# Kernel optimization log

Hardware: AMD Instinct MI355X
Metric: run time of the kernel (lower is better)

## Reference

```python
import jax, jax.numpy as jnp
import numpy as np

N = 100000
C = 128
VEC = 16
GRID = 128
TEMP = 1.0
REP = C // VEC


def _offsets_cube():
    r = [-1, 0, 1]
    return np.array([[i, j, k] for i in r for j in r for k in r], dtype=np.int64)


def _offsets_cross(d):
    offs = [[0, 0, 0]]
    for ax in range(3):
        for s in (-d, d):
            o = [0, 0, 0]
            o[ax] = s
            offs.append(o)
    return np.array(offs, dtype=np.int64)


def _build_nbr(coords, lut, offs):
    # coords [N,3] int, lut: flat grid -> voxel idx or -1. Returns [K,N] int32, -1 = missing.
    maps = []
    for o in offs:
        nc = coords + o
        valid = np.all((nc >= 0) & (nc < GRID), axis=1)
        flat = nc[:, 0] * GRID * GRID + nc[:, 1] * GRID + nc[:, 2]
        idx = np.where(valid, lut[np.clip(flat, 0, GRID ** 3 - 1)], -1)
        maps.append(idx)
    return jnp.asarray(np.stack(maps).astype(np.int32))


def setup_inputs() -> dict:
    rng = np.random.default_rng(0)
    flat = rng.choice(GRID ** 3, size=N, replace=False)
    coords = np.stack([flat // (GRID * GRID), (flat // GRID) % GRID, flat % GRID], axis=1)
    lut = np.full(GRID ** 3, -1, dtype=np.int64)
    lut[flat] = np.arange(N)
    nbr_cross2 = _build_nbr(coords, lut, _offsets_cross(2))  # expert 0: HYPER_CROSS dil=2, K=7
    nbr_cube = _build_nbr(coords, lut, _offsets_cube())       # expert 1: HYPER_CUBE dil=1, K=27
    nbr_cross3 = _build_nbr(coords, lut, _offsets_cross(3))  # expert 2: HYPER_CROSS dil=3, K=7

    ks = jax.random.split(jax.random.key(0), 10)
    s = lambda k, shape, sc: jax.random.normal(k, shape, jnp.float32) * sc
    return dict(
        x=s(ks[0], (N, C), 1.0),
        v1_w=s(ks[1], (27, C, C), 0.05),
        v1_g=jnp.ones((C,), jnp.float32), v1_b=jnp.zeros((C,), jnp.float32),
        v2_w=s(ks[2], (C, C), 0.05),
        v2_g=jnp.ones((C,), jnp.float32), v2_b=jnp.zeros((C,), jnp.float32),
        q_w=s(ks[3], (C, VEC), 0.05),
        q_g=jnp.ones((VEC,), jnp.float32), q_b=jnp.zeros((VEC,), jnp.float32),
        cb0=s(ks[4], (7, C), 0.1),
        cb1=s(ks[5], (27, C), 0.1),
        cb2=s(ks[6], (7, C), 0.1),
        out_w=s(ks[7], (C, C), 0.05),
        out_g=jnp.ones((C,), jnp.float32), out_b=jnp.zeros((C,), jnp.float32),
        nbr_cross2=nbr_cross2, nbr_cube=nbr_cube, nbr_cross3=nbr_cross3,
    )


def _bn(x, g, b, eps=1e-5):
    m = x.mean(0)
    v = x.var(0)
    return (x - m) * jax.lax.rsqrt(v + eps) * g + b


def _sparse_conv(x, nbr, W):
    # full sparse conv: out[i] = sum_k W[k] @ x[nbr[k,i]] over valid neighbors
    out = jnp.zeros((x.shape[0], W.shape[2]), x.dtype)
    for k in range(W.shape[0]):  # fixed small K, structural loop
        idx = nbr[k]
        g = jnp.where((idx >= 0)[:, None], x[jnp.clip(idx, 0)], 0.0)
        out = out + g @ W[k]
    return out


def _chanwise_conv(x, nbr, kern):
    # MinkowskiChannelwiseConvolution: out[i,c] = sum_k kern[k,c] * x[nbr[k,i],c]
    out = jnp.zeros_like(x)
    for k in range(kern.shape[0]):
        idx = nbr[k]
        out = out + jnp.where((idx >= 0)[:, None], x[jnp.clip(idx, 0)], 0.0) * kern[k]
    return out


def _pairwise_score(q, nbr):
    # pairwise qk: mean over valid neighbors j of q_i * q_j (per channel) -> [N, VEC]
    acc = jnp.zeros_like(q)
    cnt = jnp.zeros((q.shape[0], 1), q.dtype)
    for k in range(nbr.shape[0]):
        idx = nbr[k]
        valid = (idx >= 0)[:, None]
        acc = acc + jnp.where(valid, q[jnp.clip(idx, 0)], 0.0)
        cnt = cnt + valid.astype(q.dtype)
    return q * acc / jnp.maximum(cnt, 1.0)


def reference(x, v1_w, v1_g, v1_b, v2_w, v2_g, v2_b, q_w, q_g, q_b,
              cb0, cb1, cb2, out_w, out_g, out_b,
              nbr_cross2, nbr_cube, nbr_cross3):
    # value branch: 3x3 ConvBNReLU -> 1x1 ConvBNReLU
    v = jax.nn.relu(_bn(_sparse_conv(x, nbr_cube, v1_w), v1_g, v1_b))
    v = jax.nn.relu(_bn(v @ v2_w, v2_g, v2_b))
    # query: 1x1 ConvBNReLU -> [N, VEC]
    q = jax.nn.relu(_bn(x @ q_w, q_g, q_b))
    # M=3 channelwise codebook expert convs on the value features
    cb_outs = [
        _chanwise_conv(v, nbr_cross2, cb0),
        _chanwise_conv(v, nbr_cube, cb1),
        _chanwise_conv(v, nbr_cross3, cb2),
    ]
    # pairwise attention scores per expert neighborhood -> [N, VEC, M]
    scores = jnp.stack([
        _pairwise_score(q, nbr_cross2),
        _pairwise_score(q, nbr_cube),
        _pairwise_score(q, nbr_cross3),
    ], axis=-1)
    attn = jax.nn.softmax(scores / TEMP, axis=-1)
    attn = jnp.repeat(attn, REP, axis=1)  # expand_vec_dim: [N, C, M]
    out = sum(attn[:, :, m] * cb_outs[m] for m in range(3))
    out = jax.nn.relu(_bn(out @ out_w, out_g, out_b))
    return out + x  # residual (inplanes == planes, downsample is identity)
```

## Files before the change

kernel.cpp:

```cpp
#include <hip/hip_runtime.h>

#define NN 100000
#define C 128
#define VEC 16
#define AROW 136
#define GCAP 240000

typedef __bf16 bfx8 __attribute__((ext_vector_type(8)));
typedef float f32x4 __attribute__((ext_vector_type(4)));

__device__ inline unsigned pack_bf2(float a, float b) {
    unsigned ua = __float_as_uint(a);
    unsigned ub = __float_as_uint(b);
    ua = (ua + 0x7fffu + ((ua >> 16) & 1u)) >> 16;
    ub = (ub + 0x7fffu + ((ub >> 16) & 1u)) >> 16;
    return ua | (ub << 16);
}
__device__ inline unsigned short bf1(float a) {
    unsigned u = __float_as_uint(a);
    return (unsigned short)((u + 0x7fffu + ((u >> 16) & 1u)) >> 16);
}

__device__ inline void wconv_body(const float* __restrict__ W, unsigned short* __restrict__ Wf, int F) {
    int e = F & 7, l = (F >> 3) & 63, nt = (F >> 9) & 7, ks = (F >> 12) & 3, kt = F >> 14;
    int cin = ks * 32 + (l >> 4) * 8 + e;
    int cout = nt * 16 + (l & 15);
    Wf[F] = bf1(W[((size_t)kt * C + cin) * C + cout]);
}

__global__ __launch_bounds__(256) void prep(const float* __restrict__ v1w, const float* __restrict__ v2w,
                                            const float* __restrict__ outw,
                                            unsigned short* __restrict__ v1f, unsigned short* __restrict__ v2f,
                                            unsigned short* __restrict__ outf) {
    int b = blockIdx.x, tid = threadIdx.x;
    if (b < 1728)       wconv_body(v1w, v1f, b * 256 + tid);
    else if (b < 1792)  wconv_body(v2w, v2f, (b - 1728) * 256 + tid);
    else                wconv_body(outw, outf, (b - 1792) * 256 + tid);
}

__global__ __launch_bounds__(256) void compactA(const int* __restrict__ nbr, int* __restrict__ cnt,
                                                int* __restrict__ slotmap, int* __restrict__ pairs,
                                                unsigned* __restrict__ maskbuf) {
    const int k = blockIdx.x / 49, cb = blockIdx.x % 49, tid = threadIdx.x;
    const int i0 = cb * 2048 + tid * 8;
    int j[8]; int lc = 0;
#pragma unroll
    for (int t = 0; t < 8; ++t) {
        int i = i0 + t;
        j[t] = (i < NN) ? nbr[(size_t)k * NN + i] : -1;
        lc += (j[t] >= 0);
    }
    __shared__ int ls[256]; __shared__ int sbase;
    ls[tid] = lc; __syncthreads();
    for (int off = 1; off < 256; off <<= 1) {
        int v = (tid >= off) ? ls[tid - off] : 0;
        __syncthreads();
        ls[tid] += v;
        __syncthreads();
    }
    if (tid == 255) sbase = atomicAdd(&cnt[k], ls[255]);
// ... 3 lines not shown
        int i = i0 + t; if (i >= NN) break;
        int s = -1;
        if (j[t] >= 0) {
            s = slot++;
            pairs[(size_t)k * NN + s] = j[t];
            atomicOr(&maskbuf[i], 1u << k);
        }
        slotmap[(size_t)k * NN + i] = s;
    }
}

__global__ void prefixA2(int* __restrict__ hdr) {
    if (threadIdx.x == 0) {
        int co = 0, go = 0;
        for (int k = 0; k < 27; ++k) {
            hdr[32 + k] = co; hdr[64 + k] = go;
            int nch = (hdr[k] + 31) / 32;
            co += nch; go += nch * 32;
        }
        hdr[32 + 27] = co;
    }
}

__global__ __launch_bounds__(256) void convB(const float* __restrict__ x, const int* __restrict__ pairs,
                                             const int* __restrict__ hdr, const bfx8* __restrict__ Wf,
                                             unsigned short* __restrict__ g) {
    const int tid = threadIdx.x, l = tid & 63, w = tid >> 6, rr = tid >> 4, gg = tid & 15;
    __shared__ int sco[28], scnt[27], sgo[27];
    __shared__ unsigned short Ash[32 * AROW];
    __shared__ unsigned short Osh[32 * AROW];
    if (tid < 28) sco[tid] = hdr[32 + tid];
    if (tid < 27) { scnt[tid] = hdr[tid]; sgo[tid] = hdr[64 + tid]; }
    __syncthreads();
    const int tot = sco[27];
    for (int t = blockIdx.x; t < tot; t += gridDim.x) {
        int lo = 0, hi = 26;
        while (lo < hi) { int mid = (lo + hi + 1) >> 1; if (sco[mid] <= t) lo = mid; else hi = mid - 1; }
        const int k = lo, c = t - sco[k], cntk = scnt[k];
        const int srow = c * 32;
        const size_t gbase = (size_t)(sgo[k] + srow) * C;
#pragma unroll
        for (int h = 0; h < 2; ++h) {
            int row = srow + h * 16 + rr;
            uint4 pk = {0u, 0u, 0u, 0u};
            if (row < cntk) {
                int j = pairs[(size_t)k * NN + row];
                const float* xr = x + (size_t)j * C + gg * 8;
                float4 xa = *reinterpret_cast<const float4*>(xr);
                float4 xb = *reinterpret_cast<const float4*>(xr + 4);
                pk.x = pack_bf2(xa.x, xa.y); pk.y = pack_bf2(xa.z, xa.w);
                pk.z = pack_bf2(xb.x, xb.y); pk.w = pack_bf2(xb.z, xb.w);
            }
            *reinterpret_cast<uint4*>(&Ash[(h * 16 + rr) * AROW + gg * 8]) = pk;
        }
        __syncthreads();
        f32x4 a00 = {0.f,0.f,0.f,0.f}, a01 = {0.f,0.f,0.f,0.f};
        f32x4 a10 = {0.f,0.f,0.f,0.f}, a11 = {0.f,0.f,0.f,0.f};
        const unsigned short* ar0 = &Ash[(l & 15) * AROW + (l >> 4) * 8];
        const unsigned short* ar1 = &Ash[(16 + (l & 15)) * AROW + (l >> 4) * 8];
#pragma unroll
        for (int ks = 0; ks < 4; ++ks) {
            bfx8 b0 = Wf[((k * 4 + ks) * 8 + 2 * w) * 64 + l];
            bfx8 b1 = Wf[((k * 4 + ks) * 8 + 2 * w + 1) * 64 + l];
            bfx8 f0 = *reinterpret_cast<const bfx8*>(ar0 + ks * 32);
            bfx8 f1 = *reinterpret_cast<const bfx8*>(ar1 + ks * 32);
            a00 = __builtin_amdgcn_mfma_f32_16x16x32_bf16(f0, b0, a00, 0, 0, 0);
            a01 = __builtin_amdgcn_mfma_f32_16x16x32_bf16(f0, b1, a01, 0, 0, 0);
            a10 = __builtin_amdgcn_mfma_f32_16x16x32_bf16(f1, b0, a10, 0, 0, 0);
            a11 = __builtin_amdgcn_mfma_f32_16x16x32_bf16(f1, b1, a11, 0, 0, 0);
        }
#pragma unroll
        for (int r = 0; r < 4; ++r) {
            int row = (l >> 4) * 4 + r;
            Osh[row * AROW + w * 32 + (l & 15)]        = bf1(a00[r]);
// ... 30 lines not shown
        const unsigned short* gr = &g[(size_t)(sgo[k] + slot) * C + c0];
        uint4 u = *reinterpret_cast<const uint4*>(gr);
        acc[0] += __uint_as_float(u.x << 16); acc[1] += __uint_as_float(u.x & 0xffff0000u);
        acc[2] += __uint_as_float(u.y << 16); acc[3] += __uint_as_float(u.y & 0xffff0000u);
        acc[4] += __uint_as_float(u.z << 16); acc[5] += __uint_as_float(u.z & 0xffff0000u);
        acc[6] += __uint_as_float(u.w << 16); acc[7] += __uint_as_float(u.w & 0xffff0000u);
    }
#pragma unroll
    for (int c2 = 0; c2 < 8; ++c2) outt[p * 132 + c0 + c2] = acc[c2];
    uint4 pk;
    pk.x = pack_bf2(acc[0], acc[1]); pk.y = pack_bf2(acc[2], acc[3]);
    pk.z = pack_bf2(acc[4], acc[5]); pk.w = pack_bf2(acc[6], acc[7]);
    *reinterpret_cast<uint4*>(&outh[(size_t)i * C + c0]) = pk;
    __syncthreads();
    if (tid < 128) {
        float s = 0.f, q = 0.f;
#pragma unroll
        for (int r = 0; r < 16; ++r) { float v = outt[r * 132 + tid]; s += v; q += v * v; }
        psb[(size_t)blockIdx.x * C + tid] = s;
        pqb[(size_t)blockIdx.x * C + tid] = q;
    }
}

__global__ __launch_bounds__(256) void mm_bn_h(const unsigned short* __restrict__ in,
                                               const float* __restrict__ a,
                                               const float* __restrict__ cc,
                                               int dorelu,
                                               const bfx8* __restrict__ Wf,
                                               unsigned short* __restrict__ out,
                                               float* __restrict__ psb,
                                               float* __restrict__ pqb) {
    const int tid = threadIdx.x, l = tid & 63, w = tid >> 6;
    const int rr = tid >> 4, gg = tid & 15;
    const size_t base = (size_t)blockIdx.x * 16;
    __shared__ unsigned short Ash[16 * AROW];
    __shared__ float outt[16 * 132];
    {
        uint4 u = *reinterpret_cast<const uint4*>(in + (base + rr) * C + gg * 8);
        if (dorelu) {
            float4 a4 = *reinterpret_cast<const float4*>(&a[gg * 8]);
            float4 a4b = *reinterpret_cast<const float4*>(&a[gg * 8 + 4]);
            float4 c4 = *reinterpret_cast<const float4*>(&cc[gg * 8]);
            float4 c4b = *reinterpret_cast<const float4*>(&cc[gg * 8 + 4]);
            float e0 = fmaxf(fmaf(__uint_as_float(u.x << 16),        a4.x,  c4.x), 0.f);
            float e1 = fmaxf(fmaf(__uint_as_float(u.x & 0xffff0000u), a4.y,  c4.y), 0.f);
            float e2 = fmaxf(fmaf(__uint_as_float(u.y << 16),        a4.z,  c4.z), 0.f);
            float e3 = fmaxf(fmaf(__uint_as_float(u.y & 0xffff0000u), a4.w,  c4.w), 0.f);
            float e4 = fmaxf(fmaf(__uint_as_float(u.z << 16),        a4b.x, c4b.x), 0.f);
            float e5 = fmaxf(fmaf(__uint_as_float(u.z & 0xffff0000u), a4b.y, c4b.y), 0.f);
            float e6 = fmaxf(fmaf(__uint_as_float(u.w << 16),        a4b.z, c4b.z), 0.f);
            float e7 = fmaxf(fmaf(__uint_as_float(u.w & 0xffff0000u), a4b.w, c4b.w), 0.f);
            u.x = pack_bf2(e0, e1); u.y = pack_bf2(e2, e3);
            u.z = pack_bf2(e4, e5); u.w = pack_bf2(e6, e7);
        }
        *reinterpret_cast<uint4*>(&Ash[rr * AROW + gg * 8]) = u;
    }
    __syncthreads();
    f32x4 acc0 = {0.f, 0.f, 0.f, 0.f};
    f32x4 acc1 = {0.f, 0.f, 0.f, 0.f};
    const unsigned short* arow = &Ash[(l & 15) * AROW + (l >> 4) * 8];
#pragma unroll
    for (int ks = 0; ks < 4; ++ks) {
        bfx8 af = *reinterpret_cast<const bfx8*>(arow + ks * 32);
        bfx8 b0 = Wf[(ks * 8 + 2 * w) * 64 + l];
        bfx8 b1 = Wf[(ks * 8 + 2 * w + 1) * 64 + l];
        acc0 = __builtin_amdgcn_mfma_f32_16x16x32_bf16(af, b0, acc0, 0, 0, 0);
        acc1 = __builtin_amdgcn_mfma_f32_16x16x32_bf16(af, b1, acc1, 0, 0, 0);
    }
#pragma unroll
    for (int r = 0; r < 4; ++r) {
        int row = (l >> 4) * 4 + r;
        outt[row * 132 + w * 32 + (l & 15)] = acc0[r];
        outt[row * 132 + w * 32 + 16 + (l & 15)] = acc1[r];
    }
    __syncthreads();
    {
        float4 v0 = *reinterpret_cast<float4*>(&outt[rr * 132 + gg * 8]);
        float4 v1 = *reinterpret_cast<float4*>(&outt[rr * 132 + gg * 8 + 4]);
        uint4 pk;
        pk.x = pack_bf2(v0.x, v0.y); pk.y = pack_bf2(v0.z, v0.w);
        pk.z = pack_bf2(v1.x, v1.y); pk.w = pack_bf2(v1.z, v1.w);
        *reinterpret_cast<uint4*>(&out[(base + rr) * C + gg * 8]) = pk;
    }
    if (tid < 128) {
        float s = 0.f, q = 0.f;
#pragma unroll
        for (int r = 0; r < 16; ++r) { float v = outt[r * 132 + tid]; s += v; q += v * v; }
        psb[(size_t)blockIdx.x * C + tid] = s;
        pqb[(size_t)blockIdx.x * C + tid] = q;
    }
}

__global__ __launch_bounds__(256) void qmm(const float* __restrict__ x,
                                           const float* __restrict__ qw,
                                           float* __restrict__ outq) {
    const int v = threadIdx.x & 15, p = threadIdx.x >> 4;
    const size_t i = (size_t)blockIdx.x * 16 + p;
    float acc = 0.f;
    for (int cin0 = 0; cin0 < C; cin0 += 4) {
        float4 xv = *reinterpret_cast<const float4*>(x + i * C + cin0);
        acc += xv.x * qw[(cin0 + 0) * VEC + v] + xv.y * qw[(cin0 + 1) * VEC + v]
             + xv.z * qw[(cin0 + 2) * VEC + v] + xv.w * qw[(cin0 + 3) * VEC + v];
    }
    outq[i * VEC + v] = acc;
}

__global__ __launch_bounds__(256) void stats_mid128(const float* __restrict__ psb,
                                                    const float* __restrict__ pqb,
                                                    int rows,
                                                    float* __restrict__ ps2,
                                                    float* __restrict__ pq2) {
    const int ch = threadIdx.x & 127, half = threadIdx.x >> 7;
    float s = 0.f, q = 0.f;
    for (int i = blockIdx.x * 2 + half; i < rows; i += 128) {
        s += psb[(size_t)i * C + ch];
        q += pqb[(size_t)i * C + ch];
    }
    __shared__ float ls[256], lq[256];
    ls[threadIdx.x] = s; lq[threadIdx.x] = q;
    __syncthreads();
    if (threadIdx.x < 128) {
        ps2[blockIdx.x * C + ch] = ls[threadIdx.x] + ls[threadIdx.x + 128];
        pq2[blockIdx.x * C + ch] = lq[threadIdx.x] + lq[threadIdx.x + 128];
    }
}

__global__ __launch_bounds__(256) void stats_partial16(const float* __restrict__ buf,
                                                       float* __restrict__ ps,
                                                       float* __restrict__ pq) {
    const int ch = threadIdx.x & 15, grp = threadIdx.x >> 4;
    float s = 0.f, q = 0.f;
    for (int i = blockIdx.x * 16 + grp; i < NN; i += gridDim.x * 16) {
        float val = buf[(size_t)i * VEC + ch];
        s += val; q += val * val;
    }
    __shared__ float ls[256], lq[256];
    ls[threadIdx.x] = s; lq[threadIdx.x] = q;
    __syncthreads();
    if (threadIdx.x < 16) {
        float ss = 0.f, qq = 0.f;
        for (int g2 = 0; g2 < 16; ++g2) { ss += ls[g2 * 16 + ch]; qq += lq[g2 * 16 + ch]; }
        ps[blockIdx.x * VEC + ch] = ss; pq[blockIdx.x * VEC + ch] = qq;
    }
}

__global__ void stats_final(const float* __restrict__ ps, const float* __restrict__ pq,
                            int nb, int cdim,
                            const float* __restrict__ g, const float* __restrict__ b,
                            float* __restrict__ a, float* __restrict__ cc) {
    int ch = threadIdx.x;
    if (ch >= cdim) return;
    float s = 0.f, q = 0.f;
    for (int i = 0; i < nb; ++i) { s += ps[i * cdim + ch]; q += pq[i * cdim + ch]; }
    float m = s / (float)NN;
    float var = q / (float)NN - m * m;
    var = fmaxf(var, 0.f);
    float rs = rsqrtf(var + 1e-5f);
    float av = g[ch] * rs;
    a[ch] = av;
    cc[ch] = b[ch] - m * av;
}

__global__ __launch_bounds__(256) void bn_relu_ip(float* __restrict__ buf,
                                                  const float* __restrict__ a,
                                                  const float* __restrict__ cc,
                                                  int total4, int mask) {
    for (int t = blockIdx.x * blockDim.x + threadIdx.x; t < total4; t += gridDim.x * blockDim.x) {
        float4 v = reinterpret_cast<float4*>(buf)[t];
        int ch = (t * 4) & mask;
        v.x = fmaxf(fmaf(v.x, a[ch + 0], cc[ch + 0]), 0.f);
        v.y = fmaxf(fmaf(v.y, a[ch + 1], cc[ch + 1]), 0.f);
        v.z = fmaxf(fmaf(v.z, a[ch + 2], cc[ch + 2]), 0.f);
        v.w = fmaxf(fmaf(v.w, a[ch + 3], cc[ch + 3]), 0.f);
        reinterpret_cast<float4*>(buf)[t] = v;
    }
}

__global__ __launch_bounds__(256) void bnrelu_h(const unsigned short* __restrict__ in,
                                                const float* __restrict__ a,
                                                const float* __restrict__ cc,
                                                unsigned short* __restrict__ outh) {
    const int total8 = NN * C / 8;
    for (int t = blockIdx.x * 256 + threadIdx.x; t < total8; t += gridDim.x * 256) {
        int ch = (t * 8) & 127;
        uint4 u = *reinterpret_cast<const uint4*>(in + (size_t)t * 8);
        float4 a4 = *reinterpret_cast<const float4*>(&a[ch]);
        float4 a4b = *reinterpret_cast<const float4*>(&a[ch + 4]);
        float4 c4 = *reinterpret_cast<const float4*>(&cc[ch]);
        float4 c4b = *reinterpret_cast<const float4*>(&cc[ch + 4]);
        float e0 = fmaxf(fmaf(__uint_as_float(u.x << 16),        a4.x,  c4.x), 0.f);
        float e1 = fmaxf(fmaf(__uint_as_float(u.x & 0xffff0000u), a4.y,  c4.y), 0.f);
        float e2 = fmaxf(fmaf(__uint_as_float(u.y << 16),        a4.z,  c4.z), 0.f);
        float e3 = fmaxf(fmaf(__uint_as_float(u.y & 0xffff0000u), a4.w,  c4.w), 0.f);
        float e4 = fmaxf(fmaf(__uint_as_float(u.z << 16),        a4b.x, c4b.x), 0.f);
        float e5 = fmaxf(fmaf(__uint_as_float(u.z & 0xffff0000u), a4b.y, c4b.y), 0.f);
        float e6 = fmaxf(fmaf(__uint_as_float(u.w << 16),        a4b.z, c4b.z), 0.f);
        float e7 = fmaxf(fmaf(__uint_as_float(u.w & 0xffff0000u), a4b.w, c4b.w), 0.f);
        uint4 pk;
        pk.x = pack_bf2(e0, e1); pk.y = pack_bf2(e2, e3);
        pk.z = pack_bf2(e4, e5); pk.w = pack_bf2(e6, e7);
        *reinterpret_cast<uint4*>(&outh[(size_t)t * 8]) = pk;
    }
}

__global__ __launch_bounds__(256) void attn_fused16c(const unsigned short* __restrict__ vbf,
                                                     const float* __restrict__ qbuf,
                                                     const int* __restrict__ nA,
                                                     const int* __restrict__ nB,
                                                     const int* __restrict__ nC,
                                                     const float* __restrict__ cb0,
                                                     const float* __restrict__ cb1,
                                                     const float* __restrict__ cb2,
                                                     unsigned short* __restrict__ outm) {
    const int tid = threadIdx.x;
    const int base = blockIdx.x * 16;
    __shared__ int raw[16][41];
    __shared__ int sj[16][44];
    __shared__ short sk[16][44];
    __shared__ short sb[16][4];
    __shared__ float sattn[16][16][3];

    for (int t = tid; t < 656; t += 256) {
        int k = t >> 4, p = t & 15;
        int i = base + p;
        int j;
        if (k < 7)       j = nA[(size_t)k * NN + i];
        else if (k < 34) j = nB[(size_t)(k - 7) * NN + i];
        else             j = nC[(size_t)(k - 34) * NN + i];
        raw[p][k] = j;
    }
    __syncthreads();
    if (tid < 16) {
        int p = tid, n = 0;
#pragma unroll
        for (int k = 0; k < 7; ++k) { int j = raw[p][k]; if (j >= 0) { sj[p][n] = j; sk[p][n] = (short)k; ++n; } }
        int b0 = n;
#pragma unroll
        for (int k = 7; k < 34; ++k) { int j = raw[p][k]; if (j >= 0) { sj[p][n] = j; sk[p][n] = (short)(k - 7); ++n; } }
        int b1 = n;
#pragma unroll
        for (int k = 34; k < 41; ++k) { int j = raw[p][k]; if (j >= 0) { sj[p][n] = j; sk[p][n] = (short)(k - 34); ++n; } }
        sb[p][0] = (short)b0; sb[p][1] = (short)b1; sb[p][2] = (short)n;
    }
    __syncthreads();
    {
        int p = tid >> 4, v = tid & 15;
        int b0 = sb[p][0], b1 = sb[p][1], b2 = sb[p][2];
        float qi = qbuf[(size_t)(base + p) * VEC + v];
        float a0 = 0.f, a1 = 0.f, a2 = 0.f;
        for (int s = 0; s < b0; ++s) a0 += qbuf[(size_t)sj[p][s] * VEC + v];
        for (int s = b0; s < b1; ++s) a1 += qbuf[(size_t)sj[p][s] * VEC + v];
        for (int s = b1; s < b2; ++s) a2 += qbuf[(size_t)sj[p][s] * VEC + v];
        float s0 = qi * a0 / (float)(b0 > 0 ? b0 : 1);
        float s1 = qi * a1 / (float)(b1 - b0 > 0 ? b1 - b0 : 1);
        float s2 = qi * a2 / (float)(b2 - b1 > 0 ? b2 - b1 : 1);
        float mx = fmaxf(s0, fmaxf(s1, s2));
        float e0 = __expf(s0 - mx), e1 = __expf(s1 - mx), e2 = __expf(s2 - mx);
        float inv = 1.f / (e0 + e1 + e2);
        sattn[p][v][0] = e0 * inv; sattn[p][v][1] = e1 * inv; sattn[p][v][2] = e2 * inv;
    }
    __syncthreads();
    {
        int p = tid >> 4, g = tid & 15, c0 = g * 8;
        int b0 = sb[p][0], b1 = sb[p][1], b2 = sb[p][2];
        float A0[8], A1[8], A2[8];
#pragma unroll
        for (int c = 0; c < 8; ++c) { A0[c] = 0.f; A1[c] = 0.f; A2[c] = 0.f; }
        for (int s = 0; s < b0; ++s) {
            int j = sj[p][s], k = sk[p][s];
            uint4 u = *reinterpret_cast<const uint4*>(vbf + (size_t)j * C + c0);
            float4 ca = *reinterpret_cast<const float4*>(&cb0[k * C + c0]);
            float4 cb = *reinterpret_cast<const float4*>(&cb0[k * C + c0 + 4]);
            A0[0] = fmaf(ca.x, __uint_as_float(u.x << 16), A0[0]);
            A0[1] = fmaf(ca.y, __uint_as_float(u.x & 0xffff0000u), A0[1]);
            A0[2] = fmaf(ca.z, __uint_as_float(u.y << 16), A0[2]);
            A0[3] = fmaf(ca.w, __uint_as_float(u.y & 0xffff0000u), A0[3]);
            A0[4] = fmaf(cb.x, __uint_as_float(u.z << 16), A0[4]);
            A0[5] = fmaf(cb.y, __uint_as_float(u.z & 0xffff0000u), A0[5]);
            A0[6] = fmaf(cb.z, __uint_as_float(u.w << 16), A0[6]);
            A0[7] = fmaf(cb.w, __uint_as_float(u.w & 0xffff0000u), A0[7]);
        }
        for (int s = b0; s < b1; ++s) {
            int j = sj[p][s], k = sk[p][s];
            uint4 u = *reinterpret_cast<const uint4*>(vbf + (size_t)j * C + c0);
            float4 ca = *reinterpret_cast<const float4*>(&cb1[k * C + c0]);
            float4 cb = *reinterpret_cast<const float4*>(&cb1[k * C + c0 + 4]);
            A1[0] = fmaf(ca.x, __uint_as_float(u.x << 16), A1[0]);
            A1[1] = fmaf(ca.y, __uint_as_float(u.x & 0xffff0000u), A1[1]);
            A1[2] = fmaf(ca.z, __uint_as_float(u.y << 16), A1[2]);
            A1[3] = fmaf(ca.w, __uint_as_float(u.y & 0xffff0000u), A1[3]);
            A1[4] = fmaf(cb.x, __uint_as_float(u.z << 16), A1[4]);
            A1[5] = fmaf(cb.y, __uint_as_float(u.z & 0xffff0000u), A1[5]);
            A1[6] = fmaf(cb.z, __uint_as_float(u.w << 16), A1[6]);
            A1[7] = fmaf(cb.w, __uint_as_float(u.w & 0xffff0000u), A1[7]);
        }
        for (int s = b1; s < b2; ++s) {
            int j = sj[p][s], k = sk[p][s];
            uint4 u = *reinterpret_cast<const uint4*>(vbf + (size_t)j * C + c0);
            float4 ca = *reinterpret_cast<const float4*>(&cb2[k * C + c0]);
            float4 cb = *reinterpret_cast<const float4*>(&cb2[k * C + c0 + 4]);
            A2[0] = fmaf(ca.x, __uint_as_float(u.x << 16), A2[0]);
            A2[1] = fmaf(ca.y, __uint_as_float(u.x & 0xffff0000u), A2[1]);
            A2[2] = fmaf(ca.z, __uint_as_float(u.y << 16), A2[2]);
            A2[3] = fmaf(ca.w, __uint_as_float(u.y & 0xffff0000u), A2[3]);
            A2[4] = fmaf(cb.x, __uint_as_float(u.z << 16), A2[4]);
            A2[5] = fmaf(cb.y, __uint_as_float(u.z & 0xffff0000u), A2[5]);
            A2[6] = fmaf(cb.z, __uint_as_float(u.w << 16), A2[6]);
            A2[7] = fmaf(cb.w, __uint_as_float(u.w & 0xffff0000u), A2[7]);
        }
        float w0 = sattn[p][g][0], w1 = sattn[p][g][1], w2 = sattn[p][g][2];
        float o[8];
#pragma unroll
        for (int c = 0; c < 8; ++c) o[c] = w0 * A0[c] + w1 * A1[c] + w2 * A2[c];
        uint4 pk;
        pk.x = pack_bf2(o[0], o[1]); pk.y = pack_bf2(o[2], o[3]);
        pk.z = pack_bf2(o[4], o[5]); pk.w = pack_bf2(o[6], o[7]);
        *reinterpret_cast<uint4*>(&outm[(size_t)(base + p) * C + c0]) = pk;
    }
}

__global__ __launch_bounds__(256) void final_bn_res_h(const unsigned short* __restrict__ buf,
                                                      const float* __restrict__ a,
                                                      const float* __restrict__ cc,
                                                      const float* __restrict__ x,
                                                      float* __restrict__ out) {
    const int total8 = NN * C / 8;
    for (int t = blockIdx.x * 256 + threadIdx.x; t < total8; t += gridDim.x * 256) {
        int ch = (t * 8) & 127;
        uint4 u = *reinterpret_cast<const uint4*>(buf + (size_t)t * 8);
        float4 xa = *reinterpret_cast<const float4*>(x + (size_t)t * 8);
        float4 xb = *reinterpret_cast<const float4*>(x + (size_t)t * 8 + 4);
// ... 28 lines not shown
    const float* v2_b = (const float*)d_in[6];
    const float* q_w  = (const float*)d_in[7];
    const float* q_g  = (const float*)d_in[8];
    const float* q_b  = (const float*)d_in[9];
    const float* cb0  = (const float*)d_in[10];
    const float* cb1  = (const float*)d_in[11];
    const float* cb2  = (const float*)d_in[12];
    const float* out_w = (const float*)d_in[13];
    const float* out_g = (const float*)d_in[14];
    const float* out_b = (const float*)d_in[15];
    const int* nbrA = (const int*)d_in[16];
    const int* nbrB = (const int*)d_in[17];
    const int* nbrC = (const int*)d_in[18];
    float* out = (float*)d_out;

    float* w = (float*)d_ws;
    unsigned short* bufAh = (unsigned short*)w;
    float* r1 = w + (size_t)NN * C / 2;
    unsigned short* g = (unsigned short*)r1;
    int* slotmap = (int*)(r1 + 15360000);
    int* pairs   = (int*)(r1 + 15360000 + 2700000);
    unsigned short* bufBh = (unsigned short*)r1;
    float* bufQ = r1 + 6400000;
    unsigned short* vbf = (unsigned short*)(r1 + 6400000 + 1600000);
    size_t o = (size_t)NN * C / 2 + 20760000;
    float* psb  = w + o; o += (size_t)6250 * C;
    float* pqb  = w + o; o += (size_t)6250 * C;
    float* ps2  = w + o; o += 64 * C;
    float* pq2  = w + o; o += 64 * C;
    float* ps16 = w + o; o += 128 * VEC;
    float* pq16 = w + o; o += 128 * VEC;
    float* a1 = w + o; o += C;  float* c1 = w + o; o += C;
    float* a2 = w + o; o += C;  float* c2 = w + o; o += C;
    float* ao = w + o; o += C;  float* co = w + o; o += C;
    float* aq = w + o; o += VEC; float* cq = w + o; o += VEC;
    unsigned short* v1f = (unsigned short*)(w + o); o += (27 * 16384) / 2;
    unsigned short* v2f = (unsigned short*)(w + o); o += 16384 / 2;
    unsigned short* outf = (unsigned short*)(w + o); o += 16384 / 2;
    int* hdr = (int*)(w + o); o += 128;
    unsigned* maskbuf = (unsigned*)(w + o); o += NN;

    const int total4q = NN * VEC / 4;

    hipMemsetAsync(hdr, 0, (size_t)(128 + NN) * sizeof(int), stream);
    prep<<<1856, 256, 0, stream>>>(v1_w, v2_w, out_w, v1f, v2f, outf);

    compactA<<<27 * 49, 256, 0, stream>>>(nbrB, hdr, slotmap, pairs, maskbuf);
    prefixA2<<<1, 64, 0, stream>>>(hdr);
    convB<<<2048, 256, 0, stream>>>(x, pairs, hdr, (const bfx8*)v1f, g);
    convC<<<NN / 16, 256, 0, stream>>>(g, slotmap, hdr, maskbuf, bufAh, psb, pqb);
    stats_mid128<<<64, 256, 0, stream>>>(psb, pqb, 6250, ps2, pq2);
    stats_final<<<1, 128, 0, stream>>>(ps2, pq2, 64, C, v1_g, v1_b, a1, c1);

    mm_bn_h<<<NN / 16, 256, 0, stream>>>(bufAh, a1, c1, 1, (const bfx8*)v2f, bufBh, psb, pqb);
    stats_mid128<<<64, 256, 0, stream>>>(psb, pqb, 6250, ps2, pq2);
    stats_final<<<1, 128, 0, stream>>>(ps2, pq2, 64, C, v2_g, v2_b, a2, c2);

    bnrelu_h<<<2048, 256, 0, stream>>>(bufBh, a2, c2, vbf);

    qmm<<<NN / 16, 256, 0, stream>>>(x, q_w, bufQ);
    stats_partial16<<<128, 256, 0, stream>>>(bufQ, ps16, pq16);
    stats_final<<<1, 64, 0, stream>>>(ps16, pq16, 128, VEC, q_g, q_b, aq, cq);
    bn_relu_ip<<<1024, 256, 0, stream>>>(bufQ, aq, cq, total4q, 15);

    attn_fused16c<<<NN / 16, 256, 0, stream>>>(vbf, bufQ, nbrA, nbrB, nbrC, cb0, cb1, cb2, bufAh);

    mm_bn_h<<<NN / 16, 256, 0, stream>>>(bufAh, nullptr, nullptr, 0, (const bfx8*)outf, bufBh, psb, pqb);
    stats_mid128<<<64, 256, 0, stream>>>(psb, pqb, 6250, ps2, pq2);
    stats_final<<<1, 128, 0, stream>>>(ps2, pq2, 64, C, out_g, out_b, ao, co);
    final_bn_res_h<<<2048, 256, 0, stream>>>(bufBh, ao, co, x, out);
}
```

Measured before the change: 389.9 us.

## Pre-convert x to bf16, fuse BN stats finalisation, fold BN-ReLU into attention

Converts x to bf16 once inside the prep kernel, so the conv gather reads half the bytes and skips repacking on every reuse. The two-stage BN statistics reduction becomes a single kernel that uses an atomic ticket to let the last block finalise. The separate BN+ReLU passes on the value and query features are folded into the attention kernel's loads. The 1x1 matmul kernel now handles 32 rows per block, and the three expert loops in attention are merged into one loop with a branch per element. This removes several launches and full-tensor passes, at the cost of extra bf16 workspace, repeated BN math per gathered neighbour, and a divergent branch in the inner loop.

```diff
diff --git a/kernel.cpp b/kernel.cpp
--- a/kernel.cpp
+++ b/kernel.cpp
@@ -29,13 +29,24 @@
 }
 
 __global__ __launch_bounds__(256) void prep(const float* __restrict__ v1w, const float* __restrict__ v2w,
-                                            const float* __restrict__ outw,
+                                            const float* __restrict__ outw, const float* __restrict__ x,
                                             unsigned short* __restrict__ v1f, unsigned short* __restrict__ v2f,
-                                            unsigned short* __restrict__ outf) {
+                                            unsigned short* __restrict__ outf, unsigned short* __restrict__ xh) {
     int b = blockIdx.x, tid = threadIdx.x;
     if (b < 1728)       wconv_body(v1w, v1f, b * 256 + tid);
     else if (b < 1792)  wconv_body(v2w, v2f, (b - 1728) * 256 + tid);
-    else                wconv_body(outw, outf, (b - 1792) * 256 + tid);
+    else if (b < 1856)  wconv_body(outw, outf, (b - 1792) * 256 + tid);
+    else {
+        const int total8 = NN * C / 8;
+        for (int t = (b - 1856) * 256 + tid; t < total8; t += 1024 * 256) {
+            float4 xa = *reinterpret_cast<const float4*>(x + (size_t)t * 8);
+            float4 xb = *reinterpret_cast<const float4*>(x + (size_t)t * 8 + 4);
+            uint4 pk;
+            pk.x = pack_bf2(xa.x, xa.y); pk.y = pack_bf2(xa.z, xa.w);
+            pk.z = pack_bf2(xb.x, xb.y); pk.w = pack_bf2(xb.z, xb.w);
+            *reinterpret_cast<uint4*>(&xh[(size_t)t * 8]) = pk;
+        }
+    }
 }
 
 __global__ __launch_bounds__(256) void compactA(const int* __restrict__ nbr, int* __restrict__ cnt,
@@ -85,7 +96,7 @@
     }
 }
 
-__global__ __launch_bounds__(256) void convB(const float* __restrict__ x, const int* __restrict__ pairs,
+__global__ __launch_bounds__(256) void convB(const unsigned short* __restrict__ xh, const int* __restrict__ pairs,
                                              const int* __restrict__ hdr, const bfx8* __restrict__ Wf,
                                              unsigned short* __restrict__ g) {
     const int tid = threadIdx.x, l = tid & 63, w = tid >> 6, rr = tid >> 4, gg = tid & 15;
@@ -108,11 +119,7 @@
             uint4 pk = {0u, 0u, 0u, 0u};
             if (row < cntk) {
                 int j = pairs[(size_t)k * NN + row];
-                const float* xr = x + (size_t)j * C + gg * 8;
-                float4 xa = *reinterpret_cast<const float4*>(xr);
-                float4 xb = *reinterpret_cast<const float4*>(xr + 4);
-                pk.x = pack_bf2(xa.x, xa.y); pk.y = pack_bf2(xa.z, xa.w);
-                pk.z = pack_bf2(xb.x, xb.y); pk.w = pack_bf2(xb.z, xb.w);
+                pk = *reinterpret_cast<const uint4*>(xh + (size_t)j * C + gg * 8);
             }
             *reinterpret_cast<uint4*>(&Ash[(h * 16 + rr) * AROW + gg * 8]) = pk;
         }
@@ -189,21 +196,99 @@
     }
 }
 
-__global__ __launch_bounds__(256) void mm_bn_h(const unsigned short* __restrict__ in,
-                                               const float* __restrict__ a,
-                                               const float* __restrict__ cc,
-                                               int dorelu,
-                                               const bfx8* __restrict__ Wf,
-                                               unsigned short* __restrict__ out,
-                                               float* __restrict__ psb,
-                                               float* __restrict__ pqb) {
+__global__ __launch_bounds__(256) void statsF128(const float* __restrict__ psb, const float* __restrict__ pqb,
+                                                 int rows,
+                                                 float* __restrict__ ps2, float* __restrict__ pq2,
+                                                 const float* __restrict__ g, const float* __restrict__ b,
+                                                 float* __restrict__ a, float* __restrict__ cc,
+                                                 int* __restrict__ ticket) {
+    const int tid = threadIdx.x, ch = tid & 127, half = tid >> 7;
+    float s = 0.f, q = 0.f;
+    for (int i = blockIdx.x * 2 + half; i < rows; i += 128) {
+        s += psb[(size_t)i * C + ch];
+        q += pqb[(size_t)i * C + ch];
+    }
+    __shared__ float ls[256], lq[256];
+    __shared__ int amlast;
+    ls[tid] = s; lq[tid] = q;
+    __syncthreads();
+    if (tid < 128) {
+        ps2[blockIdx.x * C + ch] = ls[tid] + ls[tid + 128];
+        pq2[blockIdx.x * C + ch] = lq[tid] + lq[tid + 128];
+    }
+    __threadfence();
+    __syncthreads();
+    if (tid == 0) amlast = (atomicAdd(ticket, 1) == 63) ? 1 : 0;
+    __syncthreads();
+    if (!amlast) return;
+    __threadfence();
+    if (tid < 128) {
+        float ss = 0.f, qq = 0.f;
+        for (int i = 0; i < 64; ++i) { ss += ps2[i * C + ch]; qq += pq2[i * C + ch]; }
+        float m = ss / (float)NN;
+        float var = fmaxf(qq / (float)NN - m * m, 0.f);
+        float rs = rsqrtf(var + 1e-5f);
+        float av = g[ch] * rs;
+        a[ch] = av;
+        cc[ch] = b[ch] - m * av;
+    }
+}
+
+__global__ __launch_bounds__(256) void statsF16(const float* __restrict__ buf,
+                                                float* __restrict__ ps2, float* __restrict__ pq2,
+                                                const float* __restrict__ g, const float* __restrict__ b,
+                                                float* __restrict__ a, float* __restrict__ cc,
+                                                int* __restrict__ ticket) {
+    const int tid = threadIdx.x, ch = tid & 15, grp = tid >> 4;
+    float s = 0.f, q = 0.f;
+    for (int i = blockIdx.x * 16 + grp; i < NN; i += 64 * 16) {
+        float val = buf[(size_t)i * VEC + ch];
+        s += val; q += val * val;
+    }
+    __shared__ float ls[256], lq[256];
+    __shared__ int amlast;
+    ls[tid] = s; lq[tid] = q;
+    __syncthreads();
+    if (tid < 16) {
+        float ss = 0.f, qq = 0.f;
+        for (int g2 = 0; g2 < 16; ++g2) { ss += ls[g2 * 16 + ch]; qq += lq[g2 * 16 + ch]; }
+        ps2[blockIdx.x * VEC + ch] = ss; pq2[blockIdx.x * VEC + ch] = qq;
+    }
+    __threadfence();
+    __syncthreads();
+    if (tid == 0) amlast = (atomicAdd(ticket, 1) == 63) ? 1 : 0;
+    __syncthreads();
+    if (!amlast) return;
+    __threadfence();
+    if (tid < 16) {
+        float ss = 0.f, qq = 0.f;
+        for (int i = 0; i < 64; ++i) { ss += ps2[i * VEC + ch]; qq += pq2[i * VEC + ch]; }
+        float m = ss / (float)NN;
+        float var = fmaxf(qq / (float)NN - m * m, 0.f);
+        float rs = rsqrtf(var + 1e-5f);
+        float av = g[ch] * rs;
+        a[ch] = av;
+        cc[ch] = b[ch] - m * av;
+    }
+}
+
+__global__ __launch_bounds__(256) void mm_bn_h32(const unsigned short* __restrict__ in,
+                                                 const float* __restrict__ a,
+                                                 const float* __restrict__ cc,
+                                                 int dorelu,
+                                                 const bfx8* __restrict__ Wf,
+                                                 unsigned short* __restrict__ out,
+                                                 float* __restrict__ psb,
+                                                 float* __restrict__ pqb) {
     const int tid = threadIdx.x, l = tid & 63, w = tid >> 6;
     const int rr = tid >> 4, gg = tid & 15;
-    const size_t base = (size_t)blockIdx.x * 16;
-    __shared__ unsigned short Ash[16 * AROW];
-    __shared__ float outt[16 * 132];
-    {
-        uint4 u = *reinterpret_cast<const uint4*>(in + (base + rr) * C + gg * 8);
+    const size_t base = (size_t)blockIdx.x * 32;
+    __shared__ unsigned short Ash[32 * AROW];
+    __shared__ float outt[32 * 132];
+#pragma unroll
+    for (int h = 0; h < 2; ++h) {
+        int row = h * 16 + rr;
+        uint4 u = *reinterpret_cast<const uint4*>(in + (base + row) * C + gg * 8);
         if (dorelu) {
             float4 a4 = *reinterpret_cast<const float4*>(&a[gg * 8]);
             float4 a4b = *reinterpret_cast<const float4*>(&a[gg * 8 + 4]);
@@ -220,39 +305,47 @@
             u.x = pack_bf2(e0, e1); u.y = pack_bf2(e2, e3);
             u.z = pack_bf2(e4, e5); u.w = pack_bf2(e6, e7);
         }
-        *reinterpret_cast<uint4*>(&Ash[rr * AROW + gg * 8]) = u;
-    }
-    __syncthreads();
-    f32x4 acc0 = {0.f, 0.f, 0.f, 0.f};
-    f32x4 acc1 = {0.f, 0.f, 0.f, 0.f};
-    const unsigned short* arow = &Ash[(l & 15) * AROW + (l >> 4) * 8];
+        *reinterpret_cast<uint4*>(&Ash[row * AROW + gg * 8]) = u;
+    }
+    __syncthreads();
+    f32x4 a00 = {0.f,0.f,0.f,0.f}, a01 = {0.f,0.f,0.f,0.f};
+    f32x4 a10 = {0.f,0.f,0.f,0.f}, a11 = {0.f,0.f,0.f,0.f};
+    const unsigned short* ar0 = &Ash[(l & 15) * AROW + (l >> 4) * 8];
+    const unsigned short* ar1 = &Ash[(16 + (l & 15)) * AROW + (l >> 4) * 8];
 #pragma unroll
     for (int ks = 0; ks < 4; ++ks) {
-        bfx8 af = *reinterpret_cast<const bfx8*>(arow + ks * 32);
         bfx8 b0 = Wf[(ks * 8 + 2 * w) * 64 + l];
         bfx8 b1 = Wf[(ks * 8 + 2 * w + 1) * 64 + l];
-        acc0 = __builtin_amdgcn_mfma_f32_16x16x32_bf16(af, b0, acc0, 0, 0, 0);
-        acc1 = __builtin_amdgcn_mfma_f32_16x16x32_bf16(af, b1, acc1, 0, 0, 0);
+        bfx8 f0 = *reinterpret_cast<const bfx8*>(ar0 + ks * 32);
+        bfx8 f1 = *reinterpret_cast<const bfx8*>(ar1 + ks * 32);
+        a00 = __builtin_amdgcn_mfma_f32_16x16x32_bf16(f0, b0, a00, 0, 0, 0);
+        a01 = __builtin_amdgcn_mfma_f32_16x16x32_bf16(f0, b1, a01, 0, 0, 0);
+        a10 = __builtin_amdgcn_mfma_f32_16x16x32_bf16(f1, b0, a10, 0, 0, 0);
+        a11 = __builtin_amdgcn_mfma_f32_16x16x32_bf16(f1, b1, a11, 0, 0, 0);
     }
 #pragma unroll
     for (int r = 0; r < 4; ++r) {
         int row = (l >> 4) * 4 + r;
-        outt[row * 132 + w * 32 + (l & 15)] = acc0[r];
-        outt[row * 132 + w * 32 + 16 + (l & 15)] = acc1[r];
-    }
-    __syncthreads();
-    {
-        float4 v0 = *reinterpret_cast<float4*>(&outt[rr * 132 + gg * 8]);
-        float4 v1 = *reinterpret_cast<float4*>(&outt[rr * 132 + gg * 8 + 4]);
+        outt[row * 132 + w * 32 + (l & 15)]        = a00[r];
+        outt[row * 132 + w * 32 + 16 + (l & 15)]   = a01[r];
+        outt[(16 + row) * 132 + w * 32 + (l & 15)] = a10[r];
+        outt[(16 + row) * 132 + w * 32 + 16 + (l & 15)] = a11[r];
+    }
+    __syncthreads();
+#pragma unroll
+    for (int h = 0; h < 2; ++h) {
+        int row = h * 16 + rr;
+        float4 v0 = *reinterpret_cast<float4*>(&outt[row * 132 + gg * 8]);
+        float4 v1 = *reinterpret_cast<float4*>(&outt[row * 132 + gg * 8 + 4]);
         uint4 pk;
         pk.x = pack_bf2(v0.x, v0.y); pk.y = pack_bf2(v0.z, v0.w);
         pk.z = pack_bf2(v1.x, v1.y); pk.w = pack_bf2(v1.z, v1.w);
-        *reinterpret_cast<uint4*>(&out[(base + rr) * C + gg * 8]) = pk;
+        *reinterpret_cast<uint4*>(&out[(base + row) * C + gg * 8]) = pk;
     }
     if (tid < 128) {
         float s = 0.f, q = 0.f;
 #pragma unroll
-        for (int r = 0; r < 16; ++r) { float v = outt[r * 132 + tid]; s += v; q += v * v; }
+        for (int r = 0; r < 32; ++r) { float v = outt[r * 132 + tid]; s += v; q += v * v; }
         psb[(size_t)blockIdx.x * C + tid] = s;
         pqb[(size_t)blockIdx.x * C + tid] = q;
     }
@@ -272,106 +365,12 @@
     outq[i * VEC + v] = acc;
 }
 
-__global__ __launch_bounds__(256) void stats_mid128(const float* __restrict__ psb,
-                                                    const float* __restrict__ pqb,
-                                                    int rows,
-                                                    float* __restrict__ ps2,
-                                                    float* __restrict__ pq2) {
-    const int ch = threadIdx.x & 127, half = threadIdx.x >> 7;
-    float s = 0.f, q = 0.f;
-    for (int i = blockIdx.x * 2 + half; i < rows; i += 128) {
-        s += psb[(size_t)i * C + ch];
-        q += pqb[(size_t)i * C + ch];
-    }
-    __shared__ float ls[256], lq[256];
-    ls[threadIdx.x] = s; lq[threadIdx.x] = q;
-    __syncthreads();
-    if (threadIdx.x < 128) {
-        ps2[blockIdx.x * C + ch] = ls[threadIdx.x] + ls[threadIdx.x + 128];
-        pq2[blockIdx.x * C + ch] = lq[threadIdx.x] + lq[threadIdx.x + 128];
-    }
-}
-
-__global__ __launch_bounds__(256) void stats_partial16(const float* __restrict__ buf,
-                                                       float* __restrict__ ps,
-                                                       float* __restrict__ pq) {
-    const int ch = threadIdx.x & 15, grp = threadIdx.x >> 4;
-    float s = 0.f, q = 0.f;
-    for (int i = blockIdx.x * 16 + grp; i < NN; i += gridDim.x * 16) {
-        float val = buf[(size_t)i * VEC + ch];
-        s += val; q += val * val;
-    }
-    __shared__ float ls[256], lq[256];
-    ls[threadIdx.x] = s; lq[threadIdx.x] = q;
-    __syncthreads();
-    if (threadIdx.x < 16) {
-        float ss = 0.f, qq = 0.f;
-        for (int g2 = 0; g2 < 16; ++g2) { ss += ls[g2 * 16 + ch]; qq += lq[g2 * 16 + ch]; }
-        ps[blockIdx.x * VEC + ch] = ss; pq[blockIdx.x * VEC + ch] = qq;
-    }
-}
-
-__global__ void stats_final(const float* __restrict__ ps, const float* __restrict__ pq,
-                            int nb, int cdim,
-                            const float* __restrict__ g, const float* __restrict__ b,
-                            float* __restrict__ a, float* __restrict__ cc) {
-    int ch = threadIdx.x;
-    if (ch >= cdim) return;
-    float s = 0.f, q = 0.f;
-    for (int i = 0; i < nb; ++i) { s += ps[i * cdim + ch]; q += pq[i * cdim + ch]; }
-    float m = s / (float)NN;
-    float var = q / (float)NN - m * m;
-    var = fmaxf(var, 0.f);
-    float rs = rsqrtf(var + 1e-5f);
-    float av = g[ch] * rs;
-    a[ch] = av;
-    cc[ch] = b[ch] - m * av;
-}
-
-__global__ __launch_bounds__(256) void bn_relu_ip(float* __restrict__ buf,
-                                                  const float* __restrict__ a,
-                                                  const float* __restrict__ cc,
-                                                  int total4, int mask) {
-    for (int t = blockIdx.x * blockDim.x + threadIdx.x; t < total4; t += gridDim.x * blockDim.x) {
-        float4 v = reinterpret_cast<float4*>(buf)[t];
-        int ch = (t * 4) & mask;
-        v.x = fmaxf(fmaf(v.x, a[ch + 0], cc[ch + 0]), 0.f);
-        v.y = fmaxf(fmaf(v.y, a[ch + 1], cc[ch + 1]), 0.f);
-        v.z = fmaxf(fmaf(v.z, a[ch + 2], cc[ch + 2]), 0.f);
-        v.w = fmaxf(fmaf(v.w, a[ch + 3], cc[ch + 3]), 0.f);
-        reinterpret_cast<float4*>(buf)[t] = v;
-    }
-}
-
-__global__ __launch_bounds__(256) void bnrelu_h(const unsigned short* __restrict__ in,
-                                                const float* __restrict__ a,
-                                                const float* __restrict__ cc,
-                                                unsigned short* __restrict__ outh) {
-    const int total8 = NN * C / 8;
-    for (int t = blockIdx.x * 256 + threadIdx.x; t < total8; t += gridDim.x * 256) {
-        int ch = (t * 8) & 127;
-        uint4 u = *reinterpret_cast<const uint4*>(in + (size_t)t * 8);
-        float4 a4 = *reinterpret_cast<const float4*>(&a[ch]);
-        float4 a4b = *reinterpret_cast<const float4*>(&a[ch + 4]);
-        float4 c4 = *reinterpret_cast<const float4*>(&cc[ch]);
-        float4 c4b = *reinterpret_cast<const float4*>(&cc[ch + 4]);
-        float e0 = fmaxf(fmaf(__uint_as_float(u.x << 16),        a4.x,  c4.x), 0.f);
-        float e1 = fmaxf(fmaf(__uint_as_float(u.x & 0xffff0000u), a4.y,  c4.y), 0.f);
-        float e2 = fmaxf(fmaf(__uint_as_float(u.y << 16),        a4.z,  c4.z), 0.f);
-        float e3 = fmaxf(fmaf(__uint_as_float(u.y & 0xffff0000u), a4.w,  c4.w), 0.f);
-        float e4 = fmaxf(fmaf(__uint_as_float(u.z << 16),        a4b.x, c4b.x), 0.f);
-        float e5 = fmaxf(fmaf(__uint_as_float(u.z & 0xffff0000u), a4b.y, c4b.y), 0.f);
-        float e6 = fmaxf(fmaf(__uint_as_float(u.w << 16),        a4b.z, c4b.z), 0.f);
-        float e7 = fmaxf(fmaf(__uint_as_float(u.w & 0xffff0000u), a4b.w, c4b.w), 0.f);
-        uint4 pk;
-        pk.x = pack_bf2(e0, e1); pk.y = pack_bf2(e2, e3);
-        pk.z = pack_bf2(e4, e5); pk.w = pack_bf2(e6, e7);
-        *reinterpret_cast<uint4*>(&outh[(size_t)t * 8]) = pk;
-    }
-}
-
-__global__ __launch_bounds__(256) void attn_fused16c(const unsigned short* __restrict__ vbf,
-                                                     const float* __restrict__ qbuf,
+__global__ __launch_bounds__(256) void attn_fused16d(const unsigned short* __restrict__ vraw,
+                                                     const float* __restrict__ a2,
+                                                     const float* __restrict__ c2,
+                                                     const float* __restrict__ qraw,
+                                                     const float* __restrict__ aq,
+                                                     const float* __restrict__ cq,
                                                      const int* __restrict__ nA,
                                                      const int* __restrict__ nB,
                                                      const int* __restrict__ nC,
@@ -413,14 +412,15 @@
     {
         int p = tid >> 4, v = tid & 15;
         int b0 = sb[p][0], b1 = sb[p][1], b2 = sb[p][2];
-        float qi = qbuf[(size_t)(base + p) * VEC + v];
-        float a0 = 0.f, a1 = 0.f, a2 = 0.f;
-        for (int s = 0; s < b0; ++s) a0 += qbuf[(size_t)sj[p][s] * VEC + v];
-        for (int s = b0; s < b1; ++s) a1 += qbuf[(size_t)sj[p][s] * VEC + v];
-        for (int s = b1; s < b2; ++s) a2 += qbuf[(size_t)sj[p][s] * VEC + v];
+        float av = aq[v], cv = cq[v];
+        float qi = fmaxf(fmaf(qraw[(size_t)(base + p) * VEC + v], av, cv), 0.f);
+        float a0 = 0.f, a1 = 0.f, a2s = 0.f;
+        for (int s = 0; s < b0; ++s) a0 += fmaxf(fmaf(qraw[(size_t)sj[p][s] * VEC + v], av, cv), 0.f);
+        for (int s = b0; s < b1; ++s) a1 += fmaxf(fmaf(qraw[(size_t)sj[p][s] * VEC + v], av, cv), 0.f);
+        for (int s = b1; s < b2; ++s) a2s += fmaxf(fmaf(qraw[(size_t)sj[p][s] * VEC + v], av, cv), 0.f);
         float s0 = qi * a0 / (float)(b0 > 0 ? b0 : 1);
         float s1 = qi * a1 / (float)(b1 - b0 > 0 ? b1 - b0 : 1);
-        float s2 = qi * a2 / (float)(b2 - b1 > 0 ? b2 - b1 : 1);
+        float s2 = qi * a2s / (float)(b2 - b1 > 0 ? b2 - b1 : 1);
         float mx = fmaxf(s0, fmaxf(s1, s2));
         float e0 = __expf(s0 - mx), e1 = __expf(s1 - mx), e2 = __expf(s2 - mx);
         float inv = 1.f / (e0 + e1 + e2);
@@ -430,50 +430,36 @@
     {
         int p = tid >> 4, g = tid & 15, c0 = g * 8;
         int b0 = sb[p][0], b1 = sb[p][1], b2 = sb[p][2];
+        float4 va = *reinterpret_cast<const float4*>(&a2[c0]);
+        float4 vab = *reinterpret_cast<const float4*>(&a2[c0 + 4]);
+        float4 vc = *reinterpret_cast<const float4*>(&c2[c0]);
+        float4 vcb = *reinterpret_cast<const float4*>(&c2[c0 + 4]);
         float A0[8], A1[8], A2[8];
 #pragma unroll
         for (int c = 0; c < 8; ++c) { A0[c] = 0.f; A1[c] = 0.f; A2[c] = 0.f; }
-        for (int s = 0; s < b0; ++s) {
+        for (int s = 0; s < b2; ++s) {
             int j = sj[p][s], k = sk[p][s];
-            uint4 u = *reinterpret_cast<const uint4*>(vbf + (size_t)j * C + c0);
-            float4 ca = *reinterpret_cast<const float4*>(&cb0[k * C + c0]);
-            float4 cb = *reinterpret_cast<const float4*>(&cb0[k * C + c0 + 4]);
-            A0[0] = fmaf(ca.x, __uint_as_float(u.x << 16), A0[0]);
-            A0[1] = fmaf(ca.y, __uint_as_float(u.x & 0xffff0000u), A0[1]);
-            A0[2] = fmaf(ca.z, __uint_as_float(u.y << 16), A0[2]);
-            A0[3] = fmaf(ca.w, __uint_as_float(u.y & 0xffff0000u), A0[3]);
-            A0[4] = fmaf(cb.x, __uint_as_float(u.z << 16), A0[4]);
-            A0[5] = fmaf(cb.y, __uint_as_float(u.z & 0xffff0000u), A0[5]);
-            A0[6] = fmaf(cb.z, __uint_as_float(u.w << 16), A0[6]);
-            A0[7] = fmaf(cb.w, __uint_as_float(u.w & 0xffff0000u), A0[7]);
-        }
-        for (int s = b0; s < b1; ++s) {
-            int j = sj[p][s], k = sk[p][s];
-            uint4 u = *reinterpret_cast<const uint4*>(vbf + (size_t)j * C + c0);
-            float4 ca = *reinterpret_cast<const float4*>(&cb1[k * C + c0]);
-            float4 cb = *reinterpret_cast<const float4*>(&cb1[k * C + c0 + 4]);
-            A1[0] = fmaf(ca.x, __uint_as_float(u.x << 16), A1[0]);
-            A1[1] = fmaf(ca.y, __uint_as_float(u.x & 0xffff0000u), A1[1]);
-            A1[2] = fmaf(ca.z, __uint_as_float(u.y << 16), A1[2]);
-            A1[3] = fmaf(ca.w, __uint_as_float(u.y & 0xffff0000u), A1[3]);
-            A1[4] = fmaf(cb.x, __uint_as_float(u.z << 16), A1[4]);
-            A1[5] = fmaf(cb.y, __uint_as_float(u.z & 0xffff0000u), A1[5]);
-            A1[6] = fmaf(cb.z, __uint_as_float(u.w << 16), A1[6]);
-            A1[7] = fmaf(cb.w, __uint_as_float(u.w & 0xffff0000u), A1[7]);
-        }
-        for (int s = b1; s < b2; ++s) {
-            int j = sj[p][s], k = sk[p][s];
-            uint4 u = *reinterpret_cast<const uint4*>(vbf + (size_t)j * C + c0);
-            float4 ca = *reinterpret_cast<const float4*>(&cb2[k * C + c0]);
-            float4 cb = *reinterpret_cast<const float4*>(&cb2[k * C + c0 + 4]);
-            A2[0] = fmaf(ca.x, __uint_as_float(u.x << 16), A2[0]);
-            A2[1] = fmaf(ca.y, __uint_as_float(u.x & 0xffff0000u), A2[1]);
-            A2[2] = fmaf(ca.z, __uint_as_float(u.y << 16), A2[2]);
-            A2[3] = fmaf(ca.w, __uint_as_float(u.y & 0xffff0000u), A2[3]);
-            A2[4] = fmaf(cb.x, __uint_as_float(u.z << 16), A2[4]);
-            A2[5] = fmaf(cb.y, __uint_as_float(u.z & 0xffff0000u), A2[5]);
-            A2[6] = fmaf(cb.z, __uint_as_float(u.w << 16), A2[6]);
-            A2[7] = fmaf(cb.w, __uint_as_float(u.w & 0xffff0000u), A2[7]);
+            uint4 u = *reinterpret_cast<const uint4*>(vraw + (size_t)j * C + c0);
+            float e[8];
+            e[0] = fmaxf(fmaf(__uint_as_float(u.x << 16),        va.x,  vc.x), 0.f);
+            e[1] = fmaxf(fmaf(__uint_as_float(u.x & 0xffff0000u), va.y,  vc.y), 0.f);
+            e[2] = fmaxf(fmaf(__uint_as_float(u.y << 16),        va.z,  vc.z), 0.f);
+            e[3] = fmaxf(fmaf(__uint_as_float(u.y & 0xffff0000u), va.w,  vc.w), 0.f);
+            e[4] = fmaxf(fmaf(__uint_as_float(u.z << 16),        vab.x, vcb.x), 0.f);
+            e[5] = fmaxf(fmaf(__uint_as_float(u.z & 0xffff0000u), vab.y, vcb.y), 0.f);
+            e[6] = fmaxf(fmaf(__uint_as_float(u.w << 16),        vab.z, vcb.z), 0.f);
+            e[7] = fmaxf(fmaf(__uint_as_float(u.w & 0xffff0000u), vab.w, vcb.w), 0.f);
+            const float* cbp;
+            float* A;
+            if (s < b0)      { cbp = &cb0[k * C + c0]; A = A0; }
+            else if (s < b1) { cbp = &cb1[k * C + c0]; A = A1; }
+            else             { cbp = &cb2[k * C + c0]; A = A2; }
+            float4 ca = *reinterpret_cast<const float4*>(cbp);
+            float4 cb = *reinterpret_cast<const float4*>(cbp + 4);
+            A[0] = fmaf(ca.x, e[0], A[0]); A[1] = fmaf(ca.y, e[1], A[1]);
+            A[2] = fmaf(ca.z, e[2], A[2]); A[3] = fmaf(ca.w, e[3], A[3]);
+            A[4] = fmaf(cb.x, e[4], A[4]); A[5] = fmaf(cb.y, e[5], A[5]);
+            A[6] = fmaf(cb.z, e[6], A[6]); A[7] = fmaf(cb.w, e[7], A[7]);
         }
         float w0 = sattn[p][g][0], w1 = sattn[p][g][1], w2 = sattn[p][g][2];
         float o[8];
@@ -548,14 +534,14 @@
     int* pairs   = (int*)(r1 + 15360000 + 2700000);
     unsigned short* bufBh = (unsigned short*)r1;
     float* bufQ = r1 + 6400000;
-    unsigned short* vbf = (unsigned short*)(r1 + 6400000 + 1600000);
     size_t o = (size_t)NN * C / 2 + 20760000;
+    unsigned short* xh = (unsigned short*)(w + o); o += (size_t)NN * C / 2;
     float* psb  = w + o; o += (size_t)6250 * C;
     float* pqb  = w + o; o += (size_t)6250 * C;
     float* ps2  = w + o; o += 64 * C;
     float* pq2  = w + o; o += 64 * C;
-    float* ps16 = w + o; o += 128 * VEC;
-    float* pq16 = w + o; o += 128 * VEC;
+    float* ps16 = w + o; o += 64 * VEC;
+    float* pq16 = w + o; o += 64 * VEC;
     float* a1 = w + o; o += C;  float* c1 = w + o; o += C;
     float* a2 = w + o; o += C;  float* c2 = w + o; o += C;
     float* ao = w + o; o += C;  float* co = w + o; o += C;
@@ -566,33 +552,25 @@
     int* hdr = (int*)(w + o); o += 128;
     unsigned* maskbuf = (unsigned*)(w + o); o += NN;
 
-    const int total4q = NN * VEC / 4;
-
     hipMemsetAsync(hdr, 0, (size_t)(128 + NN) * sizeof(int), stream);
-    prep<<<1856, 256, 0, stream>>>(v1_w, v2_w, out_w, v1f, v2f, outf);
+    prep<<<2880, 256, 0, stream>>>(v1_w, v2_w, out_w, x, v1f, v2f, outf, xh);
 
     compactA<<<27 * 49, 256, 0, stream>>>(nbrB, hdr, slotmap, pairs, maskbuf);
     prefixA2<<<1, 64, 0, stream>>>(hdr);
-    convB<<<2048, 256, 0, stream>>>(x, pairs, hdr, (const bfx8*)v1f, g);
+    convB<<<2048, 256, 0, stream>>>(xh, pairs, hdr, (const bfx8*)v1f, g);
     convC<<<NN / 16, 256, 0, stream>>>(g, slotmap, hdr, maskbuf, bufAh, psb, pqb);
-    stats_mid128<<<64, 256, 0, stream>>>(psb, pqb, 6250, ps2, pq2);
-    stats_final<<<1, 128, 0, stream>>>(ps2, pq2, 64, C, v1_g, v1_b, a1, c1);
-
-    mm_bn_h<<<NN / 16, 256, 0, stream>>>(bufAh, a1, c1, 1, (const bfx8*)v2f, bufBh, psb, pqb);
-    stats_mid128<<<64, 256, 0, stream>>>(psb, pqb, 6250, ps2, pq2);
-    stats_final<<<1, 128, 0, stream>>>(ps2, pq2, 64, C, v2_g, v2_b, a2, c2);
-
-    bnrelu_h<<<2048, 256, 0, stream>>>(bufBh, a2, c2, vbf);
+    statsF128<<<64, 256, 0, stream>>>(psb, pqb, 6250, ps2, pq2, v1_g, v1_b, a1, c1, hdr + 96);
+
+    mm_bn_h32<<<NN / 32, 256, 0, stream>>>(bufAh, a1, c1, 1, (const bfx8*)v2f, bufBh, psb, pqb);
+    statsF128<<<64, 256, 0, stream>>>(psb, pqb, 3125, ps2, pq2, v2_g, v2_b, a2, c2, hdr + 97);
 
     qmm<<<NN / 16, 256, 0, stream>>>(x, q_w, bufQ);
-    stats_partial16<<<128, 256, 0, stream>>>(bufQ, ps16, pq16);
-    stats_final<<<1, 64, 0, stream>>>(ps16, pq16, 128, VEC, q_g, q_b, aq, cq);
-    bn_relu_ip<<<1024, 256, 0, stream>>>(bufQ, aq, cq, total4q, 15);
-
-    attn_fused16c<<<NN / 16, 256, 0, stream>>>(vbf, bufQ, nbrA, nbrB, nbrC, cb0, cb1, cb2, bufAh);
-
-    mm_bn_h<<<NN / 16, 256, 0, stream>>>(bufAh, nullptr, nullptr, 0, (const bfx8*)outf, bufBh, psb, pqb);
-    stats_mid128<<<64, 256, 0, stream>>>(psb, pqb, 6250, ps2, pq2);
-    stats_final<<<1, 128, 0, stream>>>(ps2, pq2, 64, C, out_g, out_b, ao, co);
+    statsF16<<<64, 256, 0, stream>>>(bufQ, ps16, pq16, q_g, q_b, aq, cq, hdr + 98);
+
+    attn_fused16d<<<NN / 16, 256, 0, stream>>>(bufBh, a2, c2, bufQ, aq, cq,
+                                               nbrA, nbrB, nbrC, cb0, cb1, cb2, bufAh);
+
+    mm_bn_h32<<<NN / 32, 256, 0, stream>>>(bufAh, nullptr, nullptr, 0, (const bfx8*)outf, bufBh, psb, pqb);
+    statsF128<<<64, 256, 0, stream>>>(psb, pqb, 3125, ps2, pq2, out_g, out_b, ao, co, hdr + 99);
     final_bn_res_h<<<2048, 256, 0, stream>>>(bufBh, ao, co, x, out);
 }
```

After: 390.7 us. About the same (+0.2%).
